# Performance work log

Measured on AMD Instinct MI355X. Metric: run time of the kernel, lower is better.

## Reference

```python
import jax, jax.numpy as jnp
import numpy as np

B, S, H = 4, 2048, 512
DEPTH, EXP = 2, 4
MAX_LR = 0.1
C = 8            # n_chunks
L = S // C       # chunk length
HE = H * EXP


def _l2norm(x, eps=1e-12):
    n = jnp.sqrt(jnp.sum(x * x, axis=-1, keepdims=True))
    return x / jnp.maximum(n, eps)


def _mem_fwd(mw1, mb1, mw2, mb2, x):
    # ResLinear: residual MLP blocks, x <- x + W2 @ silu(W1 @ x + b1) + b2
    for d in range(DEPTH):
        h = jax.nn.silu(x @ mw1[d].T + mb1[d])
        x = x + h @ mw2[d].T + mb2[d]
    return x


def setup_inputs() -> dict:
    key = jax.random.key(0)
    ks = jax.random.split(key, 9)
    s = 1.0 / np.sqrt(H)
    s2 = 1.0 / np.sqrt(HE)
    return {
        "x": jax.random.normal(ks[0], (B, S, H), jnp.float32),
        "wq": jax.random.normal(ks[1], (H, H), jnp.float32) * s, "bq": jnp.zeros((H,), jnp.float32),
        "wk": jax.random.normal(ks[2], (H, H), jnp.float32) * s, "bk": jnp.zeros((H,), jnp.float32),
        "wv": jax.random.normal(ks[3], (H, H), jnp.float32) * s, "bv": jnp.zeros((H,), jnp.float32),
        "wlr": jax.random.normal(ks[4], (1, H), jnp.float32) * s, "blr": jnp.zeros((1,), jnp.float32),
        "wf": jax.random.normal(ks[5], (1, H), jnp.float32) * s, "bf": jnp.zeros((1,), jnp.float32),
        "wm": jax.random.normal(ks[6], (1, H), jnp.float32) * s, "bm": jnp.zeros((1,), jnp.float32),
        "mw1": jax.random.normal(ks[7], (DEPTH, HE, H), jnp.float32) * s,
        "mb1": jnp.zeros((DEPTH, HE), jnp.float32),
        "mw2": jax.random.normal(ks[8], (DEPTH, H, HE), jnp.float32) * s2,
        "mb2": jnp.zeros((DEPTH, H), jnp.float32),
        "mom_w1": jnp.zeros((DEPTH, HE, H), jnp.float32),
        "mom_b1": jnp.zeros((DEPTH, HE), jnp.float32),
        "mom_w2": jnp.zeros((DEPTH, H, HE), jnp.float32),
        "mom_b2": jnp.zeros((DEPTH, H), jnp.float32),
    }


def reference(x, wq, bq, wk, bk, wv, bv, wlr, blr, wf, bf, wm, bm,
              mw1, mb1, mw2, mb2, mom_w1, mom_b1, mom_w2, mom_b2):
    # projections (non-generating path; S % C == 0 so no padding)
    q = _l2norm(x @ wq.T + bq)                            # [B,S,H]
    k = _l2norm(x @ wk.T + bk).reshape(B, C, L, H)
    v = (x @ wv.T + bv).reshape(B, C, L, H)
    lr = jax.nn.sigmoid(x @ wlr.T + blr).reshape(B, C, L, 1) * MAX_LR
    forget = jax.nn.sigmoid(x @ wf.T + bf).reshape(B, C, L, 1)
    momg = jax.nn.sigmoid(x @ wm.T + bm).reshape(B, C, L, 1)

    mem = (mw1, mb1, mw2, mb2)

    def chunk_loss(mem_params, k_c, v_c, lr_c):
        # k_c,v_c: [B,L,H]; lr_c: [B,L,1]
        preds = _mem_fwd(*mem_params, k_c)
        loss = jnp.mean((preds - v_c) ** 2, axis=-1)      # [B,L]
        return jnp.sum(loss * lr_c[..., 0])

    # per-chunk synthetic gradients of the memory MLP, then mean over chunks
    grads = jax.vmap(jax.grad(chunk_loss), in_axes=(None, 1, 1, 1))(mem, k, v, lr)
    grads = jax.tree_util.tree_map(lambda g: jnp.mean(g, axis=0), grads)

    alpha = jnp.mean(forget, axis=(1, 2, 3))              # [B] forget gate
    theta = jnp.mean(lr, axis=(1, 2, 3))                  # [B] adaptive lr
    eta = jnp.mean(momg, axis=(1, 2, 3))                  # [B] momentum gate

    def update(p, g, m):
        shp = (B,) + (1,) * p.ndim
        a, t, e = alpha.reshape(shp), theta.reshape(shp), eta.reshape(shp)
        m_b = e * m[None] - t * g[None]                   # [B,*p.shape]
        return jnp.mean(p[None] * (1.0 - a) + m_b, axis=0)

    moms = (mom_w1, mom_b1, mom_w2, mom_b2)
    new_mem = tuple(update(p, g, m) for p, g, m in zip(mem, grads, moms))

    return _mem_fwd(*new_mem, q)                          # [B,S,H]
```

## Files before the change

kernel.cpp:

```cpp
#include <hip/hip_runtime.h>
#include <cstdint>
#include <cstddef>


#define NROWS 8192
#define HDIM  512
#define HEDIM 2048
#define NCHUNK 8
#define BK    64
#define DPCOEF (2.0f / (HDIM * NCHUNK))

typedef unsigned short u16;
typedef __attribute__((ext_vector_type(8))) unsigned short u16x8;
typedef __attribute__((ext_vector_type(8))) short bf16x8;
typedef __attribute__((ext_vector_type(4))) float f32x4;

__device__ __forceinline__ float sigmoidf_(float x){ return 1.0f/(1.0f+__expf(-x)); }
__device__ __forceinline__ float siluf_(float x){ return x*sigmoidf_(x); }
__device__ __forceinline__ float dsiluf_(float x){ float s=sigmoidf_(x); return s*(1.0f+x*(1.0f-s)); }
__device__ __forceinline__ u16 bf1_(float x){
    union{float f; unsigned u;} v; v.f = x;
    return (u16)((v.u + 0x7fffu + ((v.u>>16)&1u)) >> 16);
}
__device__ __forceinline__ float bf2f_(u16 h){
    union{unsigned u; float f;} v; v.u = ((unsigned)h) << 16; return v.f;
}
__device__ __forceinline__ int swkey_(int row){
    return (((row>>3)&1)<<2) | (((row>>4)&1)<<1) | ((row>>5)&1);
}
__device__ __forceinline__ void gl_lds16(const u16* g, u16* l){
    __builtin_amdgcn_global_load_lds(
        (const __attribute__((address_space(1))) unsigned*)g,
        (__attribute__((address_space(3))) unsigned*)l, 16, 0, 0);
}

template<int MODE, bool ATR>
__global__ __launch_bounds__(256)
void mgemm_k(const u16* __restrict__ A, const u16* __restrict__ B,
             const float* __restrict__ bias, const float* __restrict__ resF,
             const u16* __restrict__ resB, const u16* __restrict__ aux,
             const float* __restrict__ vf, const float* __restrict__ lrs,
             float* __restrict__ outF, u16* __restrict__ outB, u16* __restrict__ outB2,
             int M, int N, int K, int lda, int ldb, int ldv)
{
    __shared__ __align__(128) u16 As[128*64];
    __shared__ __align__(128) u16 Bs[128*64];
    const int tid = threadIdx.x;
    const int lane = tid & 63, wvi = tid >> 6;
    const int wm = wvi >> 1, wn = wvi & 1;
    const int lr = lane & 15, lq = lane >> 4;

    const int gx = gridDim.x;
    const int nwg = gx * gridDim.y;
    int bid = blockIdx.y * gx + blockIdx.x;
    bid = (bid & 7) * (nwg >> 3) + (bid >> 3);
    const int m0 = (bid / gx) * 128, n0 = (bid % gx) * 128;

    int kbeg = 0, kend = K;
    if (MODE == 3){ const int ks = K >> 4; kbeg = blockIdx.z * ks; kend = kbeg + ks; }

    f32x4 acc[4][4];
    const f32x4 zz = {0.f,0.f,0.f,0.f};
    #pragma unroll
    for (int i = 0; i < 4; ++i)
        #pragma unroll
        for (int j = 0; j < 4; ++j) acc[i][j] = zz;

    for (int k0 = kbeg; k0 < kend; k0 += BK) {
        if (!ATR) {
            #pragma unroll
            for (int it = 0; it < 4; ++it){
                const int seg = it*4 + wvi;
                const int key = (((seg&1)<<2)|(((seg>>1)&1)<<1)|((seg>>2)&1));
                const int row = seg*8 + (lane>>3);
                const int chunk = (lane&7) ^ key;
                gl_lds16(A + (size_t)(m0+row)*lda + k0 + chunk*8, &As[seg*512]);
                gl_lds16(B + (size_t)(n0+row)*ldb + k0 + chunk*8, &Bs[seg*512]);
            }
        } else {
            #pragma unroll
            for (int r = 0; r < 2; ++r){
                const int slot = r*256 + tid;
                const int mc = slot & 15, kp = slot >> 4;
                const int chunk = kp >> 2, t = kp & 3;
                const int key = (((mc&1)<<2)|(((mc>>1)&1)<<1)|((mc>>2)&1));
                const int cs = ((chunk ^ key) << 3) + t*2;
                {
                    const u16* p = A + (size_t)(k0 + 2*kp) * lda + m0 + mc*8;
                    u16x8 e = *(const u16x8*)p;
                    u16x8 o = *(const u16x8*)(p + lda);
                    #pragma unroll
                    for (int j = 0; j < 8; ++j)
                        *(unsigned*)&As[(mc*8 + j)*64 + cs] = (unsigned)e[j] | ((unsigned)o[j] << 16);
                }
                {
                    const u16* p = B + (size_t)(k0 + 2*kp) * ldb + n0 + mc*8;
                    u16x8 e = *(const u16x8*)p;
                    u16x8 o = *(const u16x8*)(p + ldb);
                    #pragma unroll
                    for (int j = 0; j < 8; ++j)
                        *(unsigned*)&Bs[(mc*8 + j)*64 + cs] = (unsigned)e[j] | ((unsigned)o[j] << 16);
                }
            }
        }
        __syncthreads();
        #pragma unroll
        for (int ks = 0; ks < 2; ++ks) {
            bf16x8 afr[4], bfr[4];
            #pragma unroll
            for (int i = 0; i < 4; ++i){
                const int ra = wm*64 + i*16 + lr, rb = wn*64 + i*16 + lr;
                afr[i] = *(const bf16x8*)&As[ra*64 + (((ks*4 + lq) ^ swkey_(ra)) << 3)];
                bfr[i] = *(const bf16x8*)&Bs[rb*64 + (((ks*4 + lq) ^ swkey_(rb)) << 3)];
            }
            #pragma unroll
            for (int mi = 0; mi < 4; ++mi)
                #pragma unroll
                for (int ni = 0; ni < 4; ++ni)
                    acc[mi][ni] = __builtin_amdgcn_mfma_f32_16x16x32_bf16(afr[mi], bfr[ni], acc[mi][ni], 0, 0, 0);
        }
        __syncthreads();
    }

    #pragma unroll
    for (int ni = 0; ni < 4; ++ni){
        const int col = n0 + wn*64 + ni*16 + lr;
        float bv = 0.0f;
        if (MODE==0 || MODE==1 || MODE==2 || MODE==6 || MODE==7 || MODE==8 || MODE==9) bv = bias[col];
        #pragma unroll
        for (int mi = 0; mi < 4; ++mi){
            const int rbase = m0 + wm*64 + mi*16 + lq*4;
            #pragma unroll
            for (int v = 0; v < 4; ++v){
                const int row = rbase + v;
                const size_t idx = (size_t)row * N + col;
                const float o = acc[mi][ni][v];
                if (MODE == 0){ outF[idx] = o + bv; }
                else if (MODE == 1){
                    const float u = o + bv;
                    outB[idx]  = bf1_(siluf_(u));
                    outB2[idx] = bf1_(dsiluf_(u));
                }
                else if (MODE == 2){ outB[idx] = bf1_(siluf_(o + bv)); }
                else if (MODE == 3){ outB[(size_t)blockIdx.z * M * N + idx] = bf1_(o); }
                else if (MODE == 4){ outB[idx] = bf1_(o * bf2f_(aux[idx])); }
                else if (MODE == 5){ outB[idx] = bf1_(o + resF[idx]); }
                else if (MODE == 6){ const float t = o + bv + resF[idx]; outF[idx] = t; outB[idx] = bf1_(t); }
                else if (MODE == 7){ outF[idx] = o + bv + resF[idx]; }
                else if (MODE == 8){
                    const float t = o + bv + bf2f_(resB[idx]);
                    const float g = lrs[row] * DPCOEF * (t - vf[(size_t)row * ldv + col]);
                    outF[idx] = g; outB[idx] = bf1_(g);
                }
                else if (MODE == 9){ outB[idx] = bf1_(o + bv + bf2f_(resB[idx])); }
            }
        }
    }
}

__global__ __launch_bounds__(256)
void cvt_k(const float* __restrict__ in, u16* __restrict__ out, int n8)
{
    const int i = blockIdx.x * 256 + threadIdx.x;
    if (i < n8){
        const float4 a = *(const float4*)(in + (size_t)i*8);
        const float4 b = *(const float4*)(in + (size_t)i*8 + 4);
        u16x8 o;
        o[0]=bf1_(a.x); o[1]=bf1_(a.y); o[2]=bf1_(a.z); o[3]=bf1_(a.w);
        o[4]=bf1_(b.x); o[5]=bf1_(b.y); o[6]=bf1_(b.z); o[7]=bf1_(b.w);
        *(u16x8*)(out + (size_t)i*8) = o;
    }
}

__global__ __launch_bounds__(256)
void prep_kvq_k(const float* __restrict__ wk, const float* __restrict__ wv,
                const float* __restrict__ wq, const float* __restrict__ bk,
                const float* __restrict__ bv, const float* __restrict__ bq,
                u16* __restrict__ wkvqb, float* __restrict__ bkvq)
{
    const int per = HDIM*HDIM/8;
    const int id = blockIdx.x * 256 + threadIdx.x;
    if (id < 3*per){
        const float* src = (id < per) ? wk : (id < 2*per ? wv : wq);
        const int i = id - (id < per ? 0 : (id < 2*per ? per : 2*per));
        const float4 a = *(const float4*)(src + (size_t)i*8);
        const float4 b = *(const float4*)(src + (size_t)i*8 + 4);
        u16x8 o;
        o[0]=bf1_(a.x); o[1]=bf1_(a.y); o[2]=bf1_(a.z); o[3]=bf1_(a.w);
        o[4]=bf1_(b.x); o[5]=bf1_(b.y); o[6]=bf1_(b.z); o[7]=bf1_(b.w);
        *(u16x8*)(wkvqb + (size_t)id*8) = o;
    } else {
        const int j = id - 3*per;
        if (j < 3*HDIM)
            bkvq[j] = (j < HDIM) ? bk[j] : (j < 2*HDIM ? bv[j-HDIM] : bq[j-2*HDIM]);
    }
}

__global__ __launch_bounds__(256)
void tcvt_k(const float* __restrict__ in, u16* __restrict__ out, int R, int C)
{
    __shared__ float t[32][33];
    const int tx = threadIdx.x & 31, ty = threadIdx.x >> 5;
    const int c0 = blockIdx.x * 32, r0 = blockIdx.y * 32;
    #pragma unroll
    for (int j = 0; j < 4; ++j)
        t[ty + 8*j][tx] = in[(size_t)(r0 + ty + 8*j) * C + c0 + tx];
    __syncthreads();
    #pragma unroll
    for (int j = 0; j < 4; ++j)
        out[(size_t)(c0 + ty + 8*j) * R + r0 + tx] = bf1_(t[tx][ty + 8*j]);
}

template<bool WF32>
__global__ __launch_bounds__(64)
void l2norm_k(const float* __restrict__ in, int ld,
              float* __restrict__ outF, u16* __restrict__ outB)
{
    const float* p = in + (size_t)blockIdx.x * ld;
    const int t = threadIdx.x;
    float4 v0 = *(const float4*)(p + t*8), v1 = *(const float4*)(p + t*8 + 4);
    float s = v0.x*v0.x+v0.y*v0.y+v0.z*v0.z+v0.w*v0.w
            + v1.x*v1.x+v1.y*v1.y+v1.z*v1.z+v1.w*v1.w;
    #pragma unroll
    for (int o = 1; o < 64; o <<= 1) s += __shfl_xor(s, o);
    const float sc = 1.0f / fmaxf(sqrtf(s), 1e-12f);
    v0.x*=sc; v0.y*=sc; v0.z*=sc; v0.w*=sc;
    v1.x*=sc; v1.y*=sc; v1.z*=sc; v1.w*=sc;
    if (WF32){
        float* q = outF + (size_t)blockIdx.x * HDIM;
        *(float4*)(q + t*8) = v0; *(float4*)(q + t*8 + 4) = v1;
    }
    u16x8 ob;
    ob[0]=bf1_(v0.x); ob[1]=bf1_(v0.y); ob[2]=bf1_(v0.z); ob[3]=bf1_(v0.w);
    ob[4]=bf1_(v1.x); ob[5]=bf1_(v1.y); ob[6]=bf1_(v1.z); ob[7]=bf1_(v1.w);
    *(u16x8*)(outB + (size_t)blockIdx.x * HDIM + t*8) = ob;
}

__global__ __launch_bounds__(64)
void gates_k(const float* __restrict__ x,
             const float* __restrict__ wlr, const float* __restrict__ blr,
             const float* __restrict__ wf,  const float* __restrict__ bfp,
             const float* __restrict__ wm,  const float* __restrict__ bm,
             float* __restrict__ lr_s, float* __restrict__ f_s, float* __restrict__ m_s)
{
    const size_t row = blockIdx.x;
    const float* p = x + row * HDIM;
    const int t = threadIdx.x;
    float s0 = 0.f, s1 = 0.f, s2 = 0.f;
    #pragma unroll
    for (int i = 0; i < 8; i += 4){
        float4 xv = *(const float4*)(p   + t*8 + i);
        float4 a  = *(const float4*)(wlr + t*8 + i);
        float4 b  = *(const float4*)(wf  + t*8 + i);
        float4 c  = *(const float4*)(wm  + t*8 + i);
        s0 += xv.x*a.x + xv.y*a.y + xv.z*a.z + xv.w*a.w;
        s1 += xv.x*b.x + xv.y*b.y + xv.z*b.z + xv.w*b.w;
        s2 += xv.x*c.x + xv.y*c.y + xv.z*c.z + xv.w*c.w;
    }
    #pragma unroll
    for (int o = 1; o < 64; o <<= 1){
        s0 += __shfl_xor(s0, o); s1 += __shfl_xor(s1, o); s2 += __shfl_xor(s2, o);
    }
    if (t == 0){
        lr_s[row] = sigmoidf_(s0 + blr[0]) * 0.1f;
        f_s[row]  = sigmoidf_(s1 + bfp[0]);
        m_s[row]  = sigmoidf_(s2 + bm[0]);
    }
}

__global__ __launch_bounds__(256)
void scalars_k(const float* __restrict__ lr_s, const float* __restrict__ f_s,
               const float* __restrict__ m_s, float* __restrict__ sc)
{
    __shared__ float sh0[256], sh1[256], sh2[256];
    const int t = threadIdx.x;
    float s0 = 0.f, s1 = 0.f, s2 = 0.f;
    for (int i = t; i < NROWS; i += 256){ s0 += f_s[i]; s1 += lr_s[i]; s2 += m_s[i]; }
    sh0[t] = s0; sh1[t] = s1; sh2[t] = s2;
    __syncthreads();
    for (int o = 128; o > 0; o >>= 1){
        if (t < o){ sh0[t] += sh0[t+o]; sh1[t] += sh1[t+o]; sh2[t] += sh2[t+o]; }
        __syncthreads();
    }
    if (t == 0){
        sc[0] = sh0[0] / (float)NROWS;
        sc[1] = sh1[0] / (float)NROWS;
        sc[2] = sh2[0] / (float)NROWS;
    }
}

template<typename T>
__global__ __launch_bounds__(64)
void colsum_part_k(const T* __restrict__ g, float* __restrict__ part, int cols)
{
    const int c = blockIdx.x * 64 + threadIdx.x;
    const int rc = blockIdx.y;
    const T* p = g + (size_t)rc * 128 * cols + c;
    float s = 0.f;
    for (int r = 0; r < 128; ++r){
        if (sizeof(T) == 2) s += bf2f_(*(const u16*)(p + (size_t)r * cols));
        else                s += *(const float*)(p + (size_t)r * cols);
    }
    part[(size_t)rc * cols + c] = s;
}

__global__ __launch_bounds__(256)
void colsum_upd_k(const float* __restrict__ part, const float* __restrict__ p,
                  const float* __restrict__ mom, const float* __restrict__ sc,
                  float* __restrict__ nb, int cols)
{
    const int c = blockIdx.x * 256 + threadIdx.x;
    if (c < cols){
        float s = 0.f;
        for (int r = 0; r < 64; ++r) s += part[(size_t)r * cols + c];
        nb[c] = p[c] * (1.0f - sc[0]) + sc[2] * mom[c] - sc[1] * s;
    }
}

__global__ __launch_bounds__(256)
void fupdate16_k(const float* __restrict__ p, const u16* __restrict__ P,
                 const float* __restrict__ mom, const float* __restrict__ sc,
                 u16* __restrict__ nWb, int n)
{
    const int i = blockIdx.x * 256 + threadIdx.x;
    if (i < n){
        float g = 0.f;
        #pragma unroll
        for (int z = 0; z < 16; ++z) g += bf2f_(P[(size_t)z * n + i]);
        nWb[i] = bf1_(p[i] * (1.0f - sc[0]) + sc[2] * mom[i] - sc[1] * g);
    }
}

extern "C" void kernel_launch(void* const* d_in, const int* in_sizes, int n_in,
                              void* d_out, int out_size, void* d_ws, size_t ws_size,
                              hipStream_t stream)
{
    const float* x      = (const float*)d_in[0];
    const float* wq     = (const float*)d_in[1];
    const float* bq     = (const float*)d_in[2];
    const float* wk     = (const float*)d_in[3];
    const float* bk     = (const float*)d_in[4];
    const float* wv     = (const float*)d_in[5];
    const float* bv     = (const float*)d_in[6];
    const float* wlr    = (const float*)d_in[7];
    const float* blr    = (const float*)d_in[8];
    const float* wf     = (const float*)d_in[9];
    const float* bfp    = (const float*)d_in[10];
    const float* wm     = (const float*)d_in[11];
    const float* bm     = (const float*)d_in[12];
    const float* mw1    = (const float*)d_in[13];
    const float* mb1    = (const float*)d_in[14];
    const float* mw2    = (const float*)d_in[15];
    const float* mb2    = (const float*)d_in[16];
    const float* mom_w1 = (const float*)d_in[17];
    const float* mom_b1 = (const float*)d_in[18];
    const float* mom_w2 = (const float*)d_in[19];
    const float* mom_b2 = (const float*)d_in[20];
    float* out = (float*)d_out;

    char* base = (char*)d_ws;
    size_t off = 0;
    auto alloc = [&](size_t bytes)->char*{ char* p = base + off; off += (bytes + 255) & ~(size_t)255; return p; };
    const size_t NHf  = (size_t)NROWS * HDIM  * 4;
    const size_t NHb  = (size_t)NROWS * HDIM  * 2;
    const size_t NHEb = (size_t)NROWS * HEDIM * 2;
    const int    WHALF = HEDIM * HDIM;

    float* F2   = (float*)alloc(NHf);
    u16*  xb    = (u16*) alloc(NHb);
    u16*  kb    = (u16*) alloc(NHb);
    u16*  x1b   = (u16*) alloc(NHb);
    u16*  g2b   = (u16*) alloc(NHb);
    u16*  hb    = (u16*) alloc(NHEb);
    u16*  db    = (u16*) alloc(NHEb);
    u16*  dhb   = (u16*) alloc(NHEb + NHf);
    u16*  wkvqb = (u16*) alloc((size_t)3*HDIM*HDIM*2);
    float* bkvq = (float*)alloc((size_t)3*HDIM*4);
    u16*  mw1b  = (u16*) alloc((size_t)2*WHALF*2);
    u16*  mw2b  = (u16*) alloc((size_t)2*WHALF*2);
    u16*  mw2Tb = (u16*) alloc((size_t)2*WHALF*2);
    u16*  mw1T1b= (u16*) alloc((size_t)WHALF*2);
    u16*  nW1b  = (u16*) alloc((size_t)2*WHALF*2);
    u16*  nW2b  = (u16*) alloc((size_t)2*WHALF*2);
    float* cpart= (float*)alloc((size_t)64*HEDIM*4);
    float* lr_s = (float*)alloc((size_t)NROWS*4);
    float* f_s  = (float*)alloc((size_t)NROWS*4);
    float* m_s  = (float*)alloc((size_t)NROWS*4);
    float* sc   = (float*)alloc(64);
    float* nb1  = (float*)alloc((size_t)2*HEDIM*4);
    float* nb2  = (float*)alloc((size_t)2*HDIM*4);
    u16* qb  = xb;
    u16* g1b = g2b;
    float* P3 = (float*)dhb;
    float* F1 = (float*)((char*)dhb + NHEb);
    u16*  Pp  = db;

    const dim3 blk(256);
    const dim3 gKVQ (3*HDIM/128, NROWS/128);
    const dim3 gN512 (HDIM/128,  NROWS/128);
    const dim3 gN2048(HEDIM/128, NROWS/128);
    const dim3 gTN2  (HEDIM/128, HDIM/128, 16);
    const dim3 gTN1  (HDIM/128,  HEDIM/128, 16);

    const float* mw1_1 = mw1 + (size_t)WHALF;
    const float* mw2_1 = mw2 + (size_t)WHALF;

    #define GARG(Ab,Bb,bi,rF,rB,ax,vv,ll,oF,oB,oB2,M,N,K,la,lb,lv) \
        ((const u16*)(Ab),(const u16*)(Bb),(const float*)(bi),(const float*)(rF),\
         (const u16*)(rB),(const u16*)(ax),(const float*)(vv),(const float*)(ll),\
         (float*)(oF),(u16*)(oB),(u16*)(oB2),(M),(N),(K),(la),(lb),(lv))

    cvt_k<<<dim3((NROWS*HDIM/8)/256), blk, 0, stream>>>(x, xb, NROWS*HDIM/8);
    prep_kvq_k<<<dim3((3*HDIM*HDIM/8 + 3*HDIM + 255)/256), blk, 0, stream>>>(wk, wv, wq, bk, bv, bq, wkvqb, bkvq);
    cvt_k<<<dim3((2*WHALF/8)/256), blk, 0, stream>>>(mw1, mw1b, 2*WHALF/8);
    cvt_k<<<dim3((2*WHALF/8)/256), blk, 0, stream>>>(mw2, mw2b, 2*WHALF/8);
    tcvt_k<<<dim3(HEDIM/32, HDIM/32), blk, 0, stream>>>(mw2,   mw2Tb,         HDIM, HEDIM);
    tcvt_k<<<dim3(HEDIM/32, HDIM/32), blk, 0, stream>>>(mw2_1, mw2Tb + WHALF, HDIM, HEDIM);
    tcvt_k<<<dim3(HDIM/32, HEDIM/32), blk, 0, stream>>>(mw1_1, mw1T1b,        HEDIM, HDIM);
    gates_k<<<NROWS, 64, 0, stream>>>(x, wlr, blr, wf, bfp, wm, bm, lr_s, f_s, m_s);
    scalars_k<<<1, blk, 0, stream>>>(lr_s, f_s, m_s, sc);

    mgemm_k<0,false><<<gKVQ, blk, 0, stream>>>GARG(xb, wkvqb, bkvq, 0,0,0,0,0, P3, 0,0, NROWS,3*HDIM,HDIM, HDIM,HDIM, 3*HDIM);
    l2norm_k<false><<<NROWS, 64, 0, stream>>>(P3,          3*HDIM, nullptr, kb);
    l2norm_k<true ><<<NROWS, 64, 0, stream>>>(P3 + 2*HDIM, 3*HDIM, F2, qb);

    mgemm_k<2,false><<<gN2048, blk, 0, stream>>>GARG(kb, mw1b, mb1, 0,0,0,0,0, 0, hb, 0, NROWS,HEDIM,HDIM, HDIM,HDIM, HEDIM);
    mgemm_k<9,false><<<gN512, blk, 0, stream>>>GARG(hb, mw2b, mb2, 0, kb, 0,0,0, 0, x1b, 0, NROWS,HDIM,HEDIM, HEDIM,HEDIM, HDIM);
    mgemm_k<1,false><<<gN2048, blk, 0, stream>>>GARG(x1b, mw1b+WHALF, mb1+HEDIM, 0,0,0,0,0, 0, hb, db, NROWS,HEDIM,HDIM, HDIM,HDIM, HEDIM);
    mgemm_k<8,false><<<gN512, blk, 0, stream>>>GARG(hb, mw2b+WHALF, mb2+HDIM, 0, x1b, 0, P3 + HDIM, lr_s, out, g2b, 0, NROWS,HDIM,HEDIM, HEDIM,HEDIM, 3*HDIM);

    colsum_part_k<float><<<dim3(HDIM/64,64), 64, 0, stream>>>(out, cpart, HDIM);
    colsum_upd_k<<<dim3(HDIM/256), blk, 0, stream>>>(cpart, mb2+HDIM, mom_b2+HDIM, sc, nb2+HDIM, HDIM);
    mgemm_k<4,false><<<gN2048, blk, 0, stream>>>GARG(g2b, mw2Tb+WHALF, 0,0,0, db, 0,0, 0, dhb, 0, NROWS,HEDIM,HDIM, HDIM,HDIM, HEDIM);
    mgemm_k<3,true><<<gTN2, blk, 0, stream>>>GARG(g2b, hb, 0,0,0,0,0,0, 0, Pp, 0, HDIM,HEDIM,NROWS, HDIM,HEDIM, HEDIM);
    fupdate16_k<<<dim3(WHALF/256), blk, 0, stream>>>(mw2_1, Pp, mom_w2+WHALF, sc, nW2b+WHALF, WHALF);
    colsum_part_k<u16><<<dim3(HEDIM/64,64), 64, 0, stream>>>(dhb, cpart, HEDIM);
    colsum_upd_k<<<dim3(HEDIM/256), blk, 0, stream>>>(cpart, mb1+HEDIM, mom_b1+HEDIM, sc, nb1+HEDIM, HEDIM);
    mgemm_k<3,true><<<gTN1, blk, 0, stream>>>GARG(dhb, x1b, 0,0,0,0,0,0, 0, Pp, 0, HEDIM,HDIM,NROWS, HEDIM,HDIM, HDIM);
    fupdate16_k<<<dim3(WHALF/256), blk, 0, stream>>>(mw1_1, Pp, mom_w1+WHALF, sc, nW1b+WHALF, WHALF);
    mgemm_k<5,false><<<gN512, blk, 0, stream>>>GARG(dhb, mw1T1b, 0, out, 0,0,0,0, 0, g1b, 0, NROWS,HDIM,HEDIM, HEDIM,HEDIM, HDIM);

    colsum_part_k<u16><<<dim3(HDIM/64,64), 64, 0, stream>>>(g1b, cpart, HDIM);
    colsum_upd_k<<<dim3(HDIM/256), blk, 0, stream>>>(cpart, mb2, mom_b2, sc, nb2, HDIM);
    mgemm_k<1,false><<<gN2048, blk, 0, stream>>>GARG(kb, mw1b, mb1, 0,0,0,0,0, 0, hb, db, NROWS,HEDIM,HDIM, HDIM,HDIM, HEDIM);
    mgemm_k<4,false><<<gN2048, blk, 0, stream>>>GARG(g1b, mw2Tb, 0,0,0, db, 0,0, 0, dhb, 0, NROWS,HEDIM,HDIM, HDIM,HDIM, HEDIM);
    mgemm_k<3,true><<<gTN2, blk, 0, stream>>>GARG(g1b, hb, 0,0,0,0,0,0, 0, Pp, 0, HDIM,HEDIM,NROWS, HDIM,HEDIM, HEDIM);
    fupdate16_k<<<dim3(WHALF/256), blk, 0, stream>>>(mw2, Pp, mom_w2, sc, nW2b, WHALF);
    colsum_part_k<u16><<<dim3(HEDIM/64,64), 64, 0, stream>>>(dhb, cpart, HEDIM);
    colsum_upd_k<<<dim3(HEDIM/256), blk, 0, stream>>>(cpart, mb1, mom_b1, sc, nb1, HEDIM);
    mgemm_k<3,true><<<gTN1, blk, 0, stream>>>GARG(dhb, kb, 0,0,0,0,0,0, 0, Pp, 0, HEDIM,HDIM,NROWS, HEDIM,HDIM, HDIM);
    fupdate16_k<<<dim3(WHALF/256), blk, 0, stream>>>(mw1, Pp, mom_w1, sc, nW1b, WHALF);

    mgemm_k<2,false><<<gN2048, blk, 0, stream>>>GARG(qb, nW1b, nb1, 0,0,0,0,0, 0, hb, 0, NROWS,HEDIM,HDIM, HDIM,HDIM, HEDIM);
    mgemm_k<6,false><<<gN512, blk, 0, stream>>>GARG(hb, nW2b, nb2, F2, 0,0,0,0, F1, x1b, 0, NROWS,HDIM,HEDIM, HEDIM,HEDIM, HDIM);
    mgemm_k<2,false><<<gN2048, blk, 0, stream>>>GARG(x1b, nW1b+WHALF, nb1+HEDIM, 0,0,0,0,0, 0, hb, 0, NROWS,HEDIM,HDIM, HDIM,HDIM, HEDIM);
    mgemm_k<7,false><<<gN512, blk, 0, stream>>>GARG(hb, nW2b+WHALF, nb2+HDIM, F1, 0,0,0,0, out, 0,0, NROWS,HDIM,HEDIM, HEDIM,HEDIM, HDIM);

    #undef GARG
    (void)in_sizes; (void)n_in; (void)out_size; (void)ws_size;
}
```

Measured before the change: 807.7 us.

## Widen transposed GEMM loads, pack split-K partials, fuse bf16 conversion kernels

```diff
diff --git a/kernel.cpp b/kernel.cpp
--- a/kernel.cpp
+++ b/kernel.cpp
@@ -21,6 +21,12 @@
 __device__ __forceinline__ u16 bf1_(float x){
     union{float f; unsigned u;} v; v.f = x;
     return (u16)((v.u + 0x7fffu + ((v.u>>16)&1u)) >> 16);
+}
+__device__ __forceinline__ unsigned bfpack_(float a, float b){
+    union{float f; unsigned u;} ua, ub; ua.f = a; ub.f = b;
+    unsigned ra = (ua.u + 0x7fffu + ((ua.u>>16)&1u)) >> 16;
+    unsigned rb = (ub.u + 0x7fffu + ((ub.u>>16)&1u)) & 0xffff0000u;
+    return ra | rb;
 }
 __device__ __forceinline__ float bf2f_(u16 h){
     union{unsigned u; float f;} v; v.u = ((unsigned)h) << 16; return v.f;
@@ -78,28 +84,35 @@
                 gl_lds16(B + (size_t)(n0+row)*ldb + k0 + chunk*8, &Bs[seg*512]);
             }
         } else {
-            #pragma unroll
-            for (int r = 0; r < 2; ++r){
-                const int slot = r*256 + tid;
-                const int mc = slot & 15, kp = slot >> 4;
-                const int chunk = kp >> 2, t = kp & 3;
-                const int key = (((mc&1)<<2)|(((mc>>1)&1)<<1)|((mc>>2)&1));
-                const int cs = ((chunk ^ key) << 3) + t*2;
-                {
-                    const u16* p = A + (size_t)(k0 + 2*kp) * lda + m0 + mc*8;
-                    u16x8 e = *(const u16x8*)p;
-                    u16x8 o = *(const u16x8*)(p + lda);
-                    #pragma unroll
-                    for (int j = 0; j < 8; ++j)
-                        *(unsigned*)&As[(mc*8 + j)*64 + cs] = (unsigned)e[j] | ((unsigned)o[j] << 16);
+            const int mc = tid & 15, kp = tid >> 4;
+            const int key = (((mc&1)<<2)|(((mc>>1)&1)<<1)|((mc>>2)&1));
+            const int cs = ((kp >> 1) ^ key) * 8 + (kp & 1) * 4;
+            {
+                const u16* p = A + (size_t)(k0 + 4*kp) * lda + m0 + mc*8;
+                u16x8 r0 = *(const u16x8*)p;
+                u16x8 r1 = *(const u16x8*)(p + lda);
+                u16x8 r2 = *(const u16x8*)(p + 2*lda);
+                u16x8 r3 = *(const u16x8*)(p + 3*lda);
+                #pragma unroll
+                for (int j = 0; j < 8; ++j){
+                    uint2 w;
+                    w.x = (unsigned)r0[j] | ((unsigned)r1[j] << 16);
+                    w.y = (unsigned)r2[j] | ((unsigned)r3[j] << 16);
+                    *(uint2*)&As[(mc*8 + j)*64 + cs] = w;
                 }
-                {
-                    const u16* p = B + (size_t)(k0 + 2*kp) * ldb + n0 + mc*8;
-                    u16x8 e = *(const u16x8*)p;
-                    u16x8 o = *(const u16x8*)(p + ldb);
-                    #pragma unroll
-                    for (int j = 0; j < 8; ++j)
-                        *(unsigned*)&Bs[(mc*8 + j)*64 + cs] = (unsigned)e[j] | ((unsigned)o[j] << 16);
+            }
+            {
+                const u16* p = B + (size_t)(k0 + 4*kp) * ldb + n0 + mc*8;
+                u16x8 r0 = *(const u16x8*)p;
+                u16x8 r1 = *(const u16x8*)(p + ldb);
+                u16x8 r2 = *(const u16x8*)(p + 2*ldb);
+                u16x8 r3 = *(const u16x8*)(p + 3*ldb);
+                #pragma unroll
+                for (int j = 0; j < 8; ++j){
+                    uint2 w;
+                    w.x = (unsigned)r0[j] | ((unsigned)r1[j] << 16);
+                    w.y = (unsigned)r2[j] | ((unsigned)r3[j] << 16);
+                    *(uint2*)&Bs[(mc*8 + j)*64 + cs] = w;
                 }
             }
         }
@@ -122,6 +135,22 @@
         __syncthreads();
     }
 
+    if (MODE == 3){
+        unsigned* P32 = (unsigned*)outB;
+        const size_t zb = (size_t)blockIdx.z * ((size_t)M * N / 2);
+        #pragma unroll
+        for (int ni = 0; ni < 4; ++ni){
+            const int col = n0 + wn*64 + ni*16 + lr;
+            #pragma unroll
+            for (int mi = 0; mi < 4; ++mi){
+                const int pr = (m0 + wm*64 + mi*16 + lq*4) >> 1;
+                P32[zb + (size_t)pr*N + col]     = bfpack_(acc[mi][ni][0], acc[mi][ni][1]);
+                P32[zb + (size_t)(pr+1)*N + col] = bfpack_(acc[mi][ni][2], acc[mi][ni][3]);
+            }
+        }
+        return;
+    }
+
     #pragma unroll
     for (int ni = 0; ni < 4; ++ni){
         const int col = n0 + wn*64 + ni*16 + lr;
@@ -142,7 +171,6 @@
                     outB2[idx] = bf1_(dsiluf_(u));
                 }
                 else if (MODE == 2){ outB[idx] = bf1_(siluf_(o + bv)); }
-                else if (MODE == 3){ outB[(size_t)blockIdx.z * M * N + idx] = bf1_(o); }
                 else if (MODE == 4){ outB[idx] = bf1_(o * bf2f_(aux[idx])); }
                 else if (MODE == 5){ outB[idx] = bf1_(o + resF[idx]); }
                 else if (MODE == 6){ const float t = o + bv + resF[idx]; outF[idx] = t; outB[idx] = bf1_(t); }
@@ -158,42 +186,44 @@
     }
 }
 
+#define XSLOTS   (NROWS*HDIM/8)
+#define W1SLOTS  (2*HEDIM*HDIM/8)
+#define KVQSLOTS (3*HDIM*HDIM/8)
 __global__ __launch_bounds__(256)
-void cvt_k(const float* __restrict__ in, u16* __restrict__ out, int n8)
-{
-    const int i = blockIdx.x * 256 + threadIdx.x;
-    if (i < n8){
-        const float4 a = *(const float4*)(in + (size_t)i*8);
-        const float4 b = *(const float4*)(in + (size_t)i*8 + 4);
-        u16x8 o;
-        o[0]=bf1_(a.x); o[1]=bf1_(a.y); o[2]=bf1_(a.z); o[3]=bf1_(a.w);
-        o[4]=bf1_(b.x); o[5]=bf1_(b.y); o[6]=bf1_(b.z); o[7]=bf1_(b.w);
-        *(u16x8*)(out + (size_t)i*8) = o;
-    }
-}
-
-__global__ __launch_bounds__(256)
-void prep_kvq_k(const float* __restrict__ wk, const float* __restrict__ wv,
-                const float* __restrict__ wq, const float* __restrict__ bk,
-                const float* __restrict__ bv, const float* __restrict__ bq,
-                u16* __restrict__ wkvqb, float* __restrict__ bkvq)
-{
-    const int per = HDIM*HDIM/8;
+void prep_all_k(const float* __restrict__ x,  u16* __restrict__ xb,
+                const float* __restrict__ mw1, u16* __restrict__ mw1b,
+                const float* __restrict__ mw2, u16* __restrict__ mw2b,
+                const float* __restrict__ wk, const float* __restrict__ wv,
+                const float* __restrict__ wq, u16* __restrict__ wkvqb,
+                const float* __restrict__ bk, const float* __restrict__ bv,
+                const float* __restrict__ bq, float* __restrict__ bkvq)
+{
     const int id = blockIdx.x * 256 + threadIdx.x;
-    if (id < 3*per){
-        const float* src = (id < per) ? wk : (id < 2*per ? wv : wq);
-        const int i = id - (id < per ? 0 : (id < 2*per ? per : 2*per));
-        const float4 a = *(const float4*)(src + (size_t)i*8);
-        const float4 b = *(const float4*)(src + (size_t)i*8 + 4);
-        u16x8 o;
-        o[0]=bf1_(a.x); o[1]=bf1_(a.y); o[2]=bf1_(a.z); o[3]=bf1_(a.w);
-        o[4]=bf1_(b.x); o[5]=bf1_(b.y); o[6]=bf1_(b.z); o[7]=bf1_(b.w);
-        *(u16x8*)(wkvqb + (size_t)id*8) = o;
-    } else {
-        const int j = id - 3*per;
+    const int W1S = 2*HEDIM*HDIM/8;
+    const float* src; u16* dst; int i;
+    if (id < XSLOTS){ src = x; dst = xb; i = id; }
+    else if (id < XSLOTS + W1S){ src = mw1; dst = mw1b; i = id - XSLOTS; }
+    else if (id < XSLOTS + 2*W1S){ src = mw2; dst = mw2b; i = id - XSLOTS - W1S; }
+    else if (id < XSLOTS + 2*W1S + KVQSLOTS){
+        const int j = id - XSLOTS - 2*W1S;
+        const int per = HDIM*HDIM/8;
+        src = (j < per) ? wk : (j < 2*per ? wv : wq);
+        i = (j < per) ? j : (j < 2*per ? j - per : j - 2*per);
+        dst = wkvqb + (size_t)(j - i) * 8 * 0 + (size_t)j*8 - (size_t)i*8;
+        dst = wkvqb + ((size_t)j - i) * 8;
+    }
+    else {
+        const int j = id - XSLOTS - 2*W1S - KVQSLOTS;
         if (j < 3*HDIM)
             bkvq[j] = (j < HDIM) ? bk[j] : (j < 2*HDIM ? bv[j-HDIM] : bq[j-2*HDIM]);
-    }
+        return;
+    }
+    const float4 a = *(const float4*)(src + (size_t)i*8);
+    const float4 b = *(const float4*)(src + (size_t)i*8 + 4);
+    u16x8 o;
+    o[0]=bf1_(a.x); o[1]=bf1_(a.y); o[2]=bf1_(a.z); o[3]=bf1_(a.w);
+    o[4]=bf1_(b.x); o[5]=bf1_(b.y); o[6]=bf1_(b.z); o[7]=bf1_(b.w);
+    *(u16x8*)(dst + (size_t)i*8) = o;
 }
 
 __global__ __launch_bounds__(256)
@@ -318,16 +348,23 @@
 }
 
 __global__ __launch_bounds__(256)
-void fupdate16_k(const float* __restrict__ p, const u16* __restrict__ P,
-                 const float* __restrict__ mom, const float* __restrict__ sc,
-                 u16* __restrict__ nWb, int n)
+void fupdate16p_k(const float* __restrict__ p, const unsigned* __restrict__ P32,
+                  const float* __restrict__ mom, const float* __restrict__ sc,
+                  u16* __restrict__ nWb, int N, int MN2)
 {
     const int i = blockIdx.x * 256 + threadIdx.x;
-    if (i < n){
-        float g = 0.f;
+    if (i < MN2){
+        float g0 = 0.f, g1 = 0.f;
         #pragma unroll
-        for (int z = 0; z < 16; ++z) g += bf2f_(P[(size_t)z * n + i]);
-        nWb[i] = bf1_(p[i] * (1.0f - sc[0]) + sc[2] * mom[i] - sc[1] * g);
+        for (int z = 0; z < 16; ++z){
+            const unsigned w = P32[(size_t)z * MN2 + i];
+            g0 += bf2f_((u16)(w & 0xffffu));
+            g1 += bf2f_((u16)(w >> 16));
+        }
+        const int c = i & (N - 1);
+        const size_t r0 = ((size_t)(i / N) * 2) * N + c;
+        nWb[r0]     = bf1_(p[r0]     * (1.0f - sc[0]) + sc[2] * mom[r0]     - sc[1] * g0);
+        nWb[r0 + N] = bf1_(p[r0 + N] * (1.0f - sc[0]) + sc[2] * mom[r0 + N] - sc[1] * g1);
     }
 }
 
@@ -393,7 +430,7 @@
     u16* g1b = g2b;
     float* P3 = (float*)dhb;
     float* F1 = (float*)((char*)dhb + NHEb);
-    u16*  Pp  = db;
+    unsigned* Pp = (unsigned*)db;
 
     const dim3 blk(256);
     const dim3 gKVQ (3*HDIM/128, NROWS/128);
@@ -401,6 +438,7 @@
     const dim3 gN2048(HEDIM/128, NROWS/128);
     const dim3 gTN2  (HEDIM/128, HDIM/128, 16);
     const dim3 gTN1  (HDIM/128,  HEDIM/128, 16);
+    const int MN2 = WHALF / 2;
 
     const float* mw1_1 = mw1 + (size_t)WHALF;
     const float* mw2_1 = mw2 + (size_t)WHALF;
@@ -410,10 +448,11 @@
          (const u16*)(rB),(const u16*)(ax),(const float*)(vv),(const float*)(ll),\
          (float*)(oF),(u16*)(oB),(u16*)(oB2),(M),(N),(K),(la),(lb),(lv))
 
-    cvt_k<<<dim3((NROWS*HDIM/8)/256), blk, 0, stream>>>(x, xb, NROWS*HDIM/8);
-    prep_kvq_k<<<dim3((3*HDIM*HDIM/8 + 3*HDIM + 255)/256), blk, 0, stream>>>(wk, wv, wq, bk, bv, bq, wkvqb, bkvq);
-    cvt_k<<<dim3((2*WHALF/8)/256), blk, 0, stream>>>(mw1, mw1b, 2*WHALF/8);
-    cvt_k<<<dim3((2*WHALF/8)/256), blk, 0, stream>>>(mw2, mw2b, 2*WHALF/8);
+    {
+        const int nblk = (XSLOTS + 2*(2*HEDIM*HDIM/8) + KVQSLOTS)/256 + (3*HDIM + 255)/256;
+        prep_all_k<<<dim3(nblk), blk, 0, stream>>>(x, xb, mw1, mw1b, mw2, mw2b,
+                                                   wk, wv, wq, wkvqb, bk, bv, bq, bkvq);
+    }
     tcvt_k<<<dim3(HEDIM/32, HDIM/32), blk, 0, stream>>>(mw2,   mw2Tb,         HDIM, HEDIM);
     tcvt_k<<<dim3(HEDIM/32, HDIM/32), blk, 0, stream>>>(mw2_1, mw2Tb + WHALF, HDIM, HEDIM);
     tcvt_k<<<dim3(HDIM/32, HEDIM/32), blk, 0, stream>>>(mw1_1, mw1T1b,        HEDIM, HDIM);
@@ -433,11 +472,11 @@
     colsum_upd_k<<<dim3(HDIM/256), blk, 0, stream>>>(cpart, mb2+HDIM, mom_b2+HDIM, sc, nb2+HDIM, HDIM);
     mgemm_k<4,false><<<gN2048, blk, 0, stream>>>GARG(g2b, mw2Tb+WHALF, 0,0,0, db, 0,0, 0, dhb, 0, NROWS,HEDIM,HDIM, HDIM,HDIM, HEDIM);
     mgemm_k<3,true><<<gTN2, blk, 0, stream>>>GARG(g2b, hb, 0,0,0,0,0,0, 0, Pp, 0, HDIM,HEDIM,NROWS, HDIM,HEDIM, HEDIM);
-    fupdate16_k<<<dim3(WHALF/256), blk, 0, stream>>>(mw2_1, Pp, mom_w2+WHALF, sc, nW2b+WHALF, WHALF);
+    fupdate16p_k<<<dim3((MN2+255)/256), blk, 0, stream>>>(mw2_1, Pp, mom_w2+WHALF, sc, nW2b+WHALF, HEDIM, MN2);
     colsum_part_k<u16><<<dim3(HEDIM/64,64), 64, 0, stream>>>(dhb, cpart, HEDIM);
     colsum_upd_k<<<dim3(HEDIM/256), blk, 0, stream>>>(cpart, mb1+HEDIM, mom_b1+HEDIM, sc, nb1+HEDIM, HEDIM);
     mgemm_k<3,true><<<gTN1, blk, 0, stream>>>GARG(dhb, x1b, 0,0,0,0,0,0, 0, Pp, 0, HEDIM,HDIM,NROWS, HEDIM,HDIM, HDIM);
-    fupdate16_k<<<dim3(WHALF/256), blk, 0, stream>>>(mw1_1, Pp, mom_w1+WHALF, sc, nW1b+WHALF, WHALF);
+    fupdate16p_k<<<dim3((MN2+255)/256), blk, 0, stream>>>(mw1_1, Pp, mom_w1+WHALF, sc, nW1b+WHALF, HDIM, MN2);
     mgemm_k<5,false><<<gN512, blk, 0, stream>>>GARG(dhb, mw1T1b, 0, out, 0,0,0,0, 0, g1b, 0, NROWS,HDIM,HEDIM, HEDIM,HEDIM, HDIM);
 
     colsum_part_k<u16><<<dim3(HDIM/64,64), 64, 0, stream>>>(g1b, cpart, HDIM);
@@ -445,11 +484,11 @@
     mgemm_k<1,false><<<gN2048, blk, 0, stream>>>GARG(kb, mw1b, mb1, 0,0,0,0,0, 0, hb, db, NROWS,HEDIM,HDIM, HDIM,HDIM, HEDIM);
     mgemm_k<4,false><<<gN2048, blk, 0, stream>>>GARG(g1b, mw2Tb, 0,0,0, db, 0,0, 0, dhb, 0, NROWS,HEDIM,HDIM, HDIM,HDIM, HEDIM);
     mgemm_k<3,true><<<gTN2, blk, 0, stream>>>GARG(g1b, hb, 0,0,0,0,0,0, 0, Pp, 0, HDIM,HEDIM,NROWS, HDIM,HEDIM, HEDIM);
-    fupdate16_k<<<dim3(WHALF/256), blk, 0, stream>>>(mw2, Pp, mom_w2, sc, nW2b, WHALF);
+    fupdate16p_k<<<dim3((MN2+255)/256), blk, 0, stream>>>(mw2, Pp, mom_w2, sc, nW2b, HEDIM, MN2);
     colsum_part_k<u16><<<dim3(HEDIM/64,64), 64, 0, stream>>>(dhb, cpart, HEDIM);
     colsum_upd_k<<<dim3(HEDIM/256), blk, 0, stream>>>(cpart, mb1, mom_b1, sc, nb1, HEDIM);
     mgemm_k<3,true><<<gTN1, blk, 0, stream>>>GARG(dhb, kb, 0,0,0,0,0,0, 0, Pp, 0, HEDIM,HDIM,NROWS, HEDIM,HDIM, HDIM);
-    fupdate16_k<<<dim3(WHALF/256), blk, 0, stream>>>(mw1, Pp, mom_w1, sc, nW1b, WHALF);
+    fupdate16p_k<<<dim3((MN2+255)/256), blk, 0, stream>>>(mw1, Pp, mom_w1, sc, nW1b, HDIM, MN2);
 
     mgemm_k<2,false><<<gN2048, blk, 0, stream>>>GARG(qb, nW1b, nb1, 0,0,0,0,0, 0, hb, 0, NROWS,HEDIM,HDIM, HDIM,HDIM, HEDIM);
     mgemm_k<6,false><<<gN512, blk, 0, stream>>>GARG(hb, nW2b, nb2, F2, 0,0,0,0, F1, x1b, 0, NROWS,HDIM,HEDIM, HEDIM,HEDIM, HDIM);
```

Result: no change. 807.4 us (-0.0%).
